# Kernel tuning notes

Measured on AMD Instinct MI355X. Metric: run time of the kernel, lower is better.

## Reference

```python
import jax, jax.numpy as jnp
import numpy as np

B, LATENT, HIDDEN, HEAD_H, OUT = 262144, 64, 512, 64, 4
EPS = 1e-5


def _layernorm(a, g, b):
    mu = jnp.mean(a, axis=-1, keepdims=True)
    var = jnp.mean(jnp.square(a - mu), axis=-1, keepdims=True)
    return (a - mu) / jnp.sqrt(var + EPS) * g + b


def _leaky(a):
    return jnp.where(a >= 0, a, 0.2 * a)


def setup_inputs() -> dict:
    key = jax.random.key(0)
    ks = jax.random.split(key, 12)
    s = lambda fan_in: 1.0 / np.sqrt(fan_in)
    return {
        "z": jax.random.normal(ks[0], (B, LATENT), dtype=jnp.float32),
        "x": jax.random.randint(ks[1], (B,), 0, 2, dtype=jnp.int32),
        "y": jax.random.randint(ks[2], (B,), 0, 2, dtype=jnp.int32),
        # encoder params (Linear stored as [in, out])
        "W1": jax.random.normal(ks[3], (LATENT, HIDDEN), dtype=jnp.float32) * s(LATENT),
        "b1": jnp.zeros((HIDDEN,), dtype=jnp.float32),
        "g1": jnp.ones((HIDDEN,), dtype=jnp.float32),
        "beta1": jnp.zeros((HIDDEN,), dtype=jnp.float32),
        "W2": jax.random.normal(ks[4], (HIDDEN, HIDDEN), dtype=jnp.float32) * s(HIDDEN),
        "b2": jnp.zeros((HIDDEN,), dtype=jnp.float32),
        "g2": jnp.ones((HIDDEN,), dtype=jnp.float32),
        "beta2": jnp.zeros((HIDDEN,), dtype=jnp.float32),
        # 4 setting-specific heads, stacked on leading axis k = 2*x + y
        "Wh1": jax.random.normal(ks[5], (4, HIDDEN, HEAD_H), dtype=jnp.float32) * s(HIDDEN),
        "bh1": jnp.zeros((4, HEAD_H), dtype=jnp.float32),
        "Wh2": jax.random.normal(ks[6], (4, HEAD_H, OUT), dtype=jnp.float32) * s(HEAD_H),
        "bh2": jnp.zeros((4, OUT), dtype=jnp.float32),
    }


def reference(z, x, y, W1, b1, g1, beta1, W2, b2, g2, beta2, Wh1, bh1, Wh2, bh2):
    # encoder: Linear -> LayerNorm -> LeakyReLU(0.2), twice
    h = _leaky(_layernorm(z @ W1 + b1, g1, beta1))          # [B, HIDDEN]
    h = _leaky(_layernorm(h @ W2 + b2, g2, beta2))          # [B, HIDDEN]
    # all 4 heads in one pass, then per-row select (equivalent to mask routing)
    t = jax.nn.relu(jnp.einsum("bh,khd->bkd", h, Wh1) + bh1)  # [B, 4, HEAD_H]
    logits_all = jnp.einsum("bkd,kdo->bko", t, Wh2) + bh2     # [B, 4, OUT]
    k = 2 * x + y                                              # head index per row
    logits = logits_all[jnp.arange(logits_all.shape[0]), k]    # [B, OUT]
    return jax.nn.softmax(logits, axis=-1)
```

## Files before the change

### kernel.cpp

```cpp
#include <hip/hip_runtime.h>

#define MT 48
#define TS 520
#define NROWS 262144
#define EPSV 1e-5f

typedef __attribute__((ext_vector_type(8))) short short8;
typedef __attribute__((ext_vector_type(4))) float floatx4;
typedef __attribute__((ext_vector_type(2))) float floatx2;
typedef __attribute__((ext_vector_type(4))) unsigned int uintx4;
typedef __attribute__((ext_vector_type(2))) unsigned int uintx2;

__device__ __forceinline__ unsigned short f2bf(float f) {
    unsigned u = __builtin_bit_cast(unsigned, f);
    u += 0x7fff + ((u >> 16) & 1);
    return (unsigned short)(u >> 16);
}
__device__ __forceinline__ float bf2f(short s) {
    unsigned u = ((unsigned)(unsigned short)s) << 16;
    return __builtin_bit_cast(float, u);
}
__device__ __forceinline__ unsigned cvtpk(float a, float b) {
    unsigned r;
    asm("v_cvt_pk_bf16_f32 %0, %1, %2" : "=v"(r) : "v"(a), "v"(b));
    return r;
}
template<int C>
__device__ __forceinline__ float dpp_add(float v) {
    int t = __builtin_amdgcn_update_dpp(0, __builtin_bit_cast(int, v), C, 0xf, 0xf, true);
    return v + __builtin_bit_cast(float, t);
}
__device__ __forceinline__ float red16(float v) {
    v = dpp_add<0x111>(v);
    v = dpp_add<0x112>(v);
    v = dpp_add<0x114>(v);
    v = dpp_add<0x118>(v);
    return v;
}

__global__ void convert_weights(const float* __restrict__ W1, const float* __restrict__ W2,
                                const float* __restrict__ Wh1, short* __restrict__ ws) {
    int idx = blockIdx.x * 256 + threadIdx.x;
    if (idx < 32768) {
        int j = idx & 7, lane = (idx >> 3) & 63, c = idx >> 9;
        int ks = c & 1, nt = (c >> 1) & 7, w = c >> 4;
        int k = ks * 32 + (lane >> 4) * 8 + j;
        int n = w * 128 + nt * 16 + (lane & 15);
        ws[idx] = (short)f2bf(W1[k * 512 + n]);
    } else if (idx < 32768 + 262144) {
        int jdx = idx - 32768;
        int j = jdx & 7, lane = (jdx >> 3) & 63, c = jdx >> 9;
        int nt = c & 7, ks = (c >> 3) & 15, w = c >> 7;
        int kp = ks * 32 + (lane >> 4) * 8 + j;
        int k  = (kp & 0x180) + ((kp & 7) << 4) + ((kp >> 3) & 15);
        int n = w * 128 + nt * 16 + (lane & 15);
        ws[idx] = (short)f2bf(W2[k * 512 + n]);
    } else if (idx < 32768 + 262144 + 131072) {
        int jdx = idx - (32768 + 262144);
        int j = jdx & 7, lane = (jdx >> 3) & 63, c = jdx >> 9;
        int nt = c & 3, ks = (c >> 2) & 15, w = c >> 6;
        int kp = ks * 32 + (lane >> 4) * 8 + j;
        int k  = (kp & 0x180) + ((kp & 7) << 4) + ((kp >> 3) & 15);
        int col = w * 64 + nt * 16 + (lane & 15);
        int kk = col >> 6, d = col & 63;
        ws[idx] = (short)f2bf(Wh1[(kk * 512 + k) * 64 + d]);
    }
}

__global__ __launch_bounds__(256, 2) void fused_kernel(
    const float* __restrict__ z, const int* __restrict__ x, const int* __restrict__ y,
    const float* __restrict__ b1, const float* __restrict__ g1, const float* __restrict__ be1,
    const float* __restrict__ b2, const float* __restrict__ g2, const float* __restrict__ be2,
    const float* __restrict__ bh1, const float* __restrict__ Wh2, const float* __restrict__ bh2,
    const short* __restrict__ ws, float* __restrict__ out)
{
    __shared__ __align__(16) short tile[MT * TS];
    __shared__ float pstats[MT][8];
    __shared__ floatx2 rstats[MT];

    int tid  = threadIdx.x;
    int wave = tid >> 6;
    int lane = tid & 63;
    int quad = lane >> 4;
    int l16  = lane & 15;
    int blk0 = blockIdx.x * MT;
    int nslab = wave * 128;

    const short* bbase1 = ws + wave * (16 * 512) + lane * 8;
    const short* bbase2 = ws + 32768 + wave * (16 * 8 * 512) + lane * 8;
    const short* bbase3 = ws + 32768 + 262144 + wave * (16 * 4 * 512) + lane * 8;

    floatx4 acc[3][8];

#pragma unroll
    for (int mt = 0; mt < 3; mt++)
#pragma unroll
        for (int nt = 0; nt < 8; nt++) acc[mt][nt] = (floatx4){0.f, 0.f, 0.f, 0.f};

    __builtin_amdgcn_s_setprio(1);
#pragma unroll
    for (int ks = 0; ks < 2; ks++) {
        short8 afr[3];
#pragma unroll
        for (int mt = 0; mt < 3; mt++) {
            int row = blk0 + mt * 16 + l16;
            row = (row < NROWS) ? row : (NROWS - 1);
            const float* zp = z + row * 64 + ks * 32 + quad * 8;
            floatx4 f0 = *(const floatx4*)zp;
            floatx4 f1 = *(const floatx4*)(zp + 4);
            uintx4 up;
            up[0] = cvtpk(f0[0], f0[1]); up[1] = cvtpk(f0[2], f0[3]);
            up[2] = cvtpk(f1[0], f1[1]); up[3] = cvtpk(f1[2], f1[3]);
            afr[mt] = __builtin_bit_cast(short8, up);
        }
#pragma unroll
        for (int nt = 0; nt < 8; nt++) {
            short8 b = *(const short8*)(bbase1 + (nt * 2 + ks) * 512);
#pragma unroll
            for (int mt = 0; mt < 3; mt++)
                acc[mt][nt] = __builtin_amdgcn_mfma_f32_16x16x32_bf16(afr[mt], b, acc[mt][nt], 0, 0, 0);
        }
    }
    __builtin_amdgcn_s_setprio(0);

    {
#pragma unroll
        for (int nt = 0; nt < 8; nt++) {
            float bv = b1[nslab + nt * 16 + l16];
#pragma unroll
            for (int mt = 0; mt < 3; mt++)
#pragma unroll
                for (int r2 = 0; r2 < 4; r2++) acc[mt][nt][r2] += bv;
        }
        float sum[3][4] = {}, sq[3][4] = {};
#pragma unroll
        for (int mt = 0; mt < 3; mt++)
#pragma unroll
            for (int nt = 0; nt < 8; nt++)
#pragma unroll
                for (int r2 = 0; r2 < 4; r2++) {
                    float v = acc[mt][nt][r2];
                    sum[mt][r2] += v; sq[mt][r2] += v * v;
                }
#pragma unroll
        for (int mt = 0; mt < 3; mt++)
#pragma unroll
            for (int r2 = 0; r2 < 4; r2++) {
                sum[mt][r2] = red16(sum[mt][r2]);
                sq[mt][r2]  = red16(sq[mt][r2]);
            }
        if (l16 == 15) {
#pragma unroll
            for (int mt = 0; mt < 3; mt++)
#pragma unroll
                for (int r2 = 0; r2 < 4; r2++) {
                    int row = mt * 16 + quad * 4 + r2;
                    *(floatx2*)&pstats[row][wave * 2] = (floatx2){sum[mt][r2], sq[mt][r2]};
                }
        }
    }
    __syncthreads();
    if (tid < MT) {
        float s = pstats[tid][0] + pstats[tid][2] + pstats[tid][4] + pstats[tid][6];
        float q = pstats[tid][1] + pstats[tid][3] + pstats[tid][5] + pstats[tid][7];
        float mean = s * (1.f / 512.f);
        float var  = q * (1.f / 512.f) - mean * mean;
        rstats[tid] = (floatx2){mean, rsqrtf(var + EPSV)};
    }
    __syncthreads();
    {
        floatx2 st[3][4];
#pragma unroll
        for (int mt = 0; mt < 3; mt++)
#pragma unroll
            for (int r2 = 0; r2 < 4; r2++) st[mt][r2] = rstats[mt * 16 + quad * 4 + r2];
        float gv[8], bev[8];
#pragma unroll
        for (int nt = 0; nt < 8; nt++) {
            int col = nslab + nt * 16 + l16;
            gv[nt] = g1[col]; bev[nt] = be1[col];
        }
#pragma unroll
        for (int mt = 0; mt < 3; mt++)
#pragma unroll
            for (int r2 = 0; r2 < 4; r2++) {
                int row = mt * 16 + quad * 4 + r2;
                float mean = st[mt][r2][0], rstd = st[mt][r2][1];
                float f[8];
#pragma unroll
                for (int nt = 0; nt < 8; nt++) {
                    float v = (acc[mt][nt][r2] - mean) * rstd * gv[nt] + bev[nt];
                    f[nt] = fmaxf(v, 0.2f * v);
                }
                uintx4 up;
                up[0] = cvtpk(f[0], f[1]); up[1] = cvtpk(f[2], f[3]);
                up[2] = cvtpk(f[4], f[5]); up[3] = cvtpk(f[6], f[7]);
                *(uintx4*)&tile[row * TS + nslab + l16 * 8] = up;
            }
    }
    __syncthreads();

#pragma unroll
    for (int mt = 0; mt < 3; mt++)
#pragma unroll
        for (int nt = 0; nt < 8; nt++) acc[mt][nt] = (floatx4){0.f, 0.f, 0.f, 0.f};

    __builtin_amdgcn_s_setprio(1);
    for (int ks = 0; ks < 16; ks++) {
        short8 afr[3];
#pragma unroll
        for (int mt = 0; mt < 3; mt++) {
            int row = mt * 16 + l16;
            afr[mt] = *(const short8*)&tile[row * TS + ks * 32 + quad * 8];
        }
#pragma unroll
        for (int nt = 0; nt < 8; nt++) {
            short8 b = *(const short8*)(bbase2 + (ks * 8 + nt) * 512);
#pragma unroll
            for (int mt = 0; mt < 3; mt++)
                acc[mt][nt] = __builtin_amdgcn_mfma_f32_16x16x32_bf16(afr[mt], b, acc[mt][nt], 0, 0, 0);
        }
    }
    __builtin_amdgcn_s_setprio(0);
    {
#pragma unroll
        for (int nt = 0; nt < 8; nt++) {
            float bv = b2[nslab + nt * 16 + l16];
#pragma unroll
            for (int mt = 0; mt < 3; mt++)
#pragma unroll
                for (int r2 = 0; r2 < 4; r2++) acc[mt][nt][r2] += bv;
        }
        float sum[3][4] = {}, sq[3][4] = {};
#pragma unroll
        for (int mt = 0; mt < 3; mt++)
#pragma unroll
            for (int nt = 0; nt < 8; nt++)
#pragma unroll
                for (int r2 = 0; r2 < 4; r2++) {
                    float v = acc[mt][nt][r2];
                    sum[mt][r2] += v; sq[mt][r2] += v * v;
                }
#pragma unroll
        for (int mt = 0; mt < 3; mt++)
#pragma unroll
            for (int r2 = 0; r2 < 4; r2++) {
                sum[mt][r2] = red16(sum[mt][r2]);
                sq[mt][r2]  = red16(sq[mt][r2]);
            }
        if (l16 == 15) {
#pragma unroll
            for (int mt = 0; mt < 3; mt++)
#pragma unroll
                for (int r2 = 0; r2 < 4; r2++) {
                    int row = mt * 16 + quad * 4 + r2;
                    *(floatx2*)&pstats[row][wave * 2] = (floatx2){sum[mt][r2], sq[mt][r2]};
                }
        }
    }
    __syncthreads();
    if (tid < MT) {
        float s = pstats[tid][0] + pstats[tid][2] + pstats[tid][4] + pstats[tid][6];
        float q = pstats[tid][1] + pstats[tid][3] + pstats[tid][5] + pstats[tid][7];
        float mean = s * (1.f / 512.f);
        float var  = q * (1.f / 512.f) - mean * mean;
        rstats[tid] = (floatx2){mean, rsqrtf(var + EPSV)};
    }
    __syncthreads();
    {
        floatx2 st[3][4];
#pragma unroll
        for (int mt = 0; mt < 3; mt++)
#pragma unroll
            for (int r2 = 0; r2 < 4; r2++) st[mt][r2] = rstats[mt * 16 + quad * 4 + r2];
        float gv[8], bev[8];
#pragma unroll
        for (int nt = 0; nt < 8; nt++) {
            int col = nslab + nt * 16 + l16;
            gv[nt] = g2[col]; bev[nt] = be2[col];
        }
#pragma unroll
        for (int mt = 0; mt < 3; mt++)
#pragma unroll
            for (int r2 = 0; r2 < 4; r2++) {
                int row = mt * 16 + quad * 4 + r2;
                float mean = st[mt][r2][0], rstd = st[mt][r2][1];
                float f[8];
#pragma unroll
                for (int nt = 0; nt < 8; nt++) {
                    float v = (acc[mt][nt][r2] - mean) * rstd * gv[nt] + bev[nt];
                    f[nt] = fmaxf(v, 0.2f * v);
                }
                uintx4 up;
                up[0] = cvtpk(f[0], f[1]); up[1] = cvtpk(f[2], f[3]);
                up[2] = cvtpk(f[4], f[5]); up[3] = cvtpk(f[6], f[7]);
                *(uintx4*)&tile[row * TS + nslab + l16 * 8] = up;
            }
    }
    __syncthreads();

#pragma unroll
    for (int mt = 0; mt < 3; mt++)
#pragma unroll
        for (int nt = 0; nt < 4; nt++) acc[mt][nt] = (floatx4){0.f, 0.f, 0.f, 0.f};

    __builtin_amdgcn_s_setprio(1);
    for (int ks = 0; ks < 16; ks++) {
        short8 afr[3];
#pragma unroll
        for (int mt = 0; mt < 3; mt++) {
            int row = mt * 16 + l16;
            afr[mt] = *(const short8*)&tile[row * TS + ks * 32 + quad * 8];
        }
#pragma unroll
        for (int nt = 0; nt < 4; nt++) {
            short8 b = *(const short8*)(bbase3 + (ks * 4 + nt) * 512);
#pragma unroll
            for (int mt = 0; mt < 3; mt++)
                acc[mt][nt] = __builtin_amdgcn_mfma_f32_16x16x32_bf16(afr[mt], b, acc[mt][nt], 0, 0, 0);
        }
    }
    __builtin_amdgcn_s_setprio(0);
    __syncthreads();
    {
        float bh1v[4];
#pragma unroll
        for (int nt = 0; nt < 4; nt++) bh1v[nt] = bh1[wave * 64 + nt * 16 + l16];
#pragma unroll
        for (int mt = 0; mt < 3; mt++)
#pragma unroll
            for (int r2 = 0; r2 < 4; r2++) {
                int row = mt * 16 + quad * 4 + r2;
                float f[4];
#pragma unroll
                for (int nt = 0; nt < 4; nt++) {
                    float v = acc[mt][nt][r2] + bh1v[nt];
                    f[nt] = (v > 0.f) ? v : 0.f;
                }
                uintx2 up = {cvtpk(f[0], f[1]), cvtpk(f[2], f[3])};
                *(uintx2*)&tile[row * TS + wave * 64 + l16 * 4] = up;
            }
    }
    __syncthreads();

    {
        int r = tid >> 2, is = tid & 3;
        if (r < MT) {
            int grow = blk0 + r;
            int gsafe = (grow < NROWS) ? grow : (NROWS - 1);
            int kk = 2 * x[gsafe] + y[gsafe];
            const short* tp = &tile[r * TS + kk * 64 + is * 16];
            short8 ta = *(const short8*)tp;
            short8 tb = *(const short8*)(tp + 8);
            const float* wp = Wh2 + kk * 256;
            float lg0 = 0.f, lg1 = 0.f, lg2 = 0.f, lg3 = 0.f;
#pragma unroll
            for (int e = 0; e < 8; e++) {
                int d0 = (e & 3) * 16 + 4 * is + (e >> 2);
                float t0 = bf2f(ta[e]);
                floatx4 w0 = *(const floatx4*)(wp + d0 * 4);
                float t1 = bf2f(tb[e]);
                floatx4 w1 = *(const floatx4*)(wp + (d0 + 2) * 4);
                lg0 += t0 * w0[0] + t1 * w1[0];
                lg1 += t0 * w0[1] + t1 * w1[1];
                lg2 += t0 * w0[2] + t1 * w1[2];
                lg3 += t0 * w0[3] + t1 * w1[3];
            }
#pragma unroll
            for (int off = 1; off < 4; off <<= 1) {
                lg0 += __shfl_xor(lg0, off, 64);
                lg1 += __shfl_xor(lg1, off, 64);
                lg2 += __shfl_xor(lg2, off, 64);
                lg3 += __shfl_xor(lg3, off, 64);
            }
            if (is == 0 && grow < NROWS) {
                lg0 += bh2[kk * 4 + 0]; lg1 += bh2[kk * 4 + 1];
                lg2 += bh2[kk * 4 + 2]; lg3 += bh2[kk * 4 + 3];
                float m = fmaxf(fmaxf(lg0, lg1), fmaxf(lg2, lg3));
                float e0 = __expf(lg0 - m), e1 = __expf(lg1 - m);
                float e2 = __expf(lg2 - m), e3 = __expf(lg3 - m);
                float inv = 1.f / (e0 + e1 + e2 + e3);
                floatx4 o = {e0 * inv, e1 * inv, e2 * inv, e3 * inv};
                *(floatx4*)(out + grow * 4) = o;
            }
        }
    }
}

extern "C" void kernel_launch(void* const* d_in, const int* in_sizes, int n_in,
                              void* d_out, int out_size, void* d_ws, size_t ws_size,
                              hipStream_t stream) {
    const float* z   = (const float*)d_in[0];
    const int*   x   = (const int*)d_in[1];
    const int*   y   = (const int*)d_in[2];
    const float* W1  = (const float*)d_in[3];
    const float* b1  = (const float*)d_in[4];
    const float* g1  = (const float*)d_in[5];
    const float* be1 = (const float*)d_in[6];
    const float* W2  = (const float*)d_in[7];
    const float* b2  = (const float*)d_in[8];
    const float* g2  = (const float*)d_in[9];
    const float* be2 = (const float*)d_in[10];
    const float* Wh1 = (const float*)d_in[11];
    const float* bh1 = (const float*)d_in[12];
    const float* Wh2 = (const float*)d_in[13];
    const float* bh2 = (const float*)d_in[14];
    short* ws = (short*)d_ws;
    float* out = (float*)d_out;

    hipLaunchKernelGGL(convert_weights, dim3(1664), dim3(256), 0, stream, W1, W2, Wh1, ws);
    hipLaunchKernelGGL(fused_kernel, dim3((NROWS + MT - 1) / MT), dim3(256), 0, stream,
                       z, x, y, b1, g1, be1, b2, g2, be2, bh1, Wh2, bh2,
                       (const short*)ws, out);
}
```

Baseline: 401.0 us.

## Restructure fused MLP so each wave owns full rows with LDS-staged shared weights

The kernel is reorganised so each of 8 waves owns 16 rows across all 512 columns, with 128 rows per 512-thread block. Weights are streamed through a double-buffered LDS buffer using global_load_lds, and that buffer is shared by all waves. LayerNorm statistics are now reduced within a wave, which removes the cross-wave pstats/rstats synchronisation, and epilogue math uses packed f32 instructions with an XOR-swizzled per-wave scratch layout. This cuts the global weight traffic per row and the block-level barriers for stats. In exchange it adds a __syncthreads per weight chunk, needs 128 accumulator VGPRs per thread, and drops the bounds guards because it assumes NROWS is divisible by 128.

```diff
diff --git a/kernel.cpp b/kernel.cpp
--- a/kernel.cpp
+++ b/kernel.cpp
@@ -1,15 +1,15 @@
 #include <hip/hip_runtime.h>
 
-#define MT 48
-#define TS 520
 #define NROWS 262144
+#define MT 128
+#define NBLK (NROWS / MT)
 #define EPSV 1e-5f
 
 typedef __attribute__((ext_vector_type(8))) short short8;
+typedef __attribute__((ext_vector_type(4))) short shortx4;
 typedef __attribute__((ext_vector_type(4))) float floatx4;
 typedef __attribute__((ext_vector_type(2))) float floatx2;
 typedef __attribute__((ext_vector_type(4))) unsigned int uintx4;
-typedef __attribute__((ext_vector_type(2))) unsigned int uintx2;
 
 __device__ __forceinline__ unsigned short f2bf(float f) {
     unsigned u = __builtin_bit_cast(unsigned, f);
@@ -24,6 +24,15 @@
     unsigned r;
     asm("v_cvt_pk_bf16_f32 %0, %1, %2" : "=v"(r) : "v"(a), "v"(b));
     return r;
+}
+__device__ __forceinline__ floatx2 pk_add(floatx2 a, floatx2 b) {
+    floatx2 d; asm("v_pk_add_f32 %0, %1, %2" : "=v"(d) : "v"(a), "v"(b)); return d;
+}
+__device__ __forceinline__ floatx2 pk_mul(floatx2 a, floatx2 b) {
+    floatx2 d; asm("v_pk_mul_f32 %0, %1, %2" : "=v"(d) : "v"(a), "v"(b)); return d;
+}
+__device__ __forceinline__ floatx2 pk_fma(floatx2 a, floatx2 b, floatx2 c) {
+    floatx2 d; asm("v_pk_fma_f32 %0, %1, %2, %3" : "=v"(d) : "v"(a), "v"(b), "v"(c)); return d;
 }
 template<int C>
 __device__ __forceinline__ float dpp_add(float v) {
@@ -37,352 +46,314 @@
     v = dpp_add<0x118>(v);
     return v;
 }
+__device__ __forceinline__ float bcast15(float v) {
+    return __builtin_bit_cast(float,
+        __builtin_amdgcn_ds_swizzle(__builtin_bit_cast(int, v), 0x01F0));
+}
+__device__ __forceinline__ void gload16(const short* g, short* l) {
+    __builtin_amdgcn_global_load_lds(
+        (const __attribute__((address_space(1))) unsigned int*)g,
+        (__attribute__((address_space(3))) unsigned int*)l, 16, 0, 0);
+}
 
 __global__ void convert_weights(const float* __restrict__ W1, const float* __restrict__ W2,
                                 const float* __restrict__ Wh1, short* __restrict__ ws) {
     int idx = blockIdx.x * 256 + threadIdx.x;
     if (idx < 32768) {
         int j = idx & 7, lane = (idx >> 3) & 63, c = idx >> 9;
-        int ks = c & 1, nt = (c >> 1) & 7, w = c >> 4;
-        int k = ks * 32 + (lane >> 4) * 8 + j;
-        int n = w * 128 + nt * 16 + (lane & 15);
+        int ntl = c & 7, ks = (c >> 3) & 1, ncg = c >> 4;
+        int q = lane >> 4, l16 = lane & 15;
+        int k = ks * 32 + q * 8 + j;
+        int n = ncg * 128 + ntl * 16 + l16;
         ws[idx] = (short)f2bf(W1[k * 512 + n]);
     } else if (idx < 32768 + 262144) {
         int jdx = idx - 32768;
         int j = jdx & 7, lane = (jdx >> 3) & 63, c = jdx >> 9;
-        int nt = c & 7, ks = (c >> 3) & 15, w = c >> 7;
-        int kp = ks * 32 + (lane >> 4) * 8 + j;
-        int k  = (kp & 0x180) + ((kp & 7) << 4) + ((kp >> 3) & 15);
-        int n = w * 128 + nt * 16 + (lane & 15);
+        int ntl = c & 7, ks = (c >> 3) & 15, ncg = c >> 7;
+        int q = lane >> 4, l16 = lane & 15;
+        int k = (q * 8 + j) * 16 + ks;
+        int n = ncg * 128 + ntl * 16 + l16;
         ws[idx] = (short)f2bf(W2[k * 512 + n]);
     } else if (idx < 32768 + 262144 + 131072) {
         int jdx = idx - (32768 + 262144);
         int j = jdx & 7, lane = (jdx >> 3) & 63, c = jdx >> 9;
-        int nt = c & 3, ks = (c >> 2) & 15, w = c >> 6;
-        int kp = ks * 32 + (lane >> 4) * 8 + j;
-        int k  = (kp & 0x180) + ((kp & 7) << 4) + ((kp >> 3) & 15);
-        int col = w * 64 + nt * 16 + (lane & 15);
-        int kk = col >> 6, d = col & 63;
-        ws[idx] = (short)f2bf(Wh1[(kk * 512 + k) * 64 + d]);
-    }
-}
-
-__global__ __launch_bounds__(256, 2) void fused_kernel(
+        int ntl = c & 7, ks = (c >> 3) & 15, ncg = c >> 7;
+        int q = lane >> 4, l16 = lane & 15;
+        int k = (q * 8 + j) * 16 + ks;
+        int d = ncg * 128 + ntl * 16 + l16;
+        int kk = d >> 6, dd = d & 63;
+        ws[idx] = (short)f2bf(Wh1[(kk * 512 + k) * 64 + dd]);
+    }
+}
+
+__global__ __launch_bounds__(512, 2) void fused_kernel(
     const float* __restrict__ z, const int* __restrict__ x, const int* __restrict__ y,
     const float* __restrict__ b1, const float* __restrict__ g1, const float* __restrict__ be1,
     const float* __restrict__ b2, const float* __restrict__ g2, const float* __restrict__ be2,
     const float* __restrict__ bh1, const float* __restrict__ Wh2, const float* __restrict__ bh2,
     const short* __restrict__ ws, float* __restrict__ out)
 {
-    __shared__ __align__(16) short tile[MT * TS];
-    __shared__ float pstats[MT][8];
-    __shared__ floatx2 rstats[MT];
+    __shared__ __align__(16) short scr[8 * 16 * 512];
+    __shared__ __align__(16) short bbuf[2][8 * 512];
 
     int tid  = threadIdx.x;
     int wave = tid >> 6;
     int lane = tid & 63;
     int quad = lane >> 4;
     int l16  = lane & 15;
-    int blk0 = blockIdx.x * MT;
-    int nslab = wave * 128;
-
-    const short* bbase1 = ws + wave * (16 * 512) + lane * 8;
-    const short* bbase2 = ws + 32768 + wave * (16 * 8 * 512) + lane * 8;
-    const short* bbase3 = ws + 32768 + 262144 + wave * (16 * 4 * 512) + lane * 8;
-
-    floatx4 acc[3][8];
-
-#pragma unroll
-    for (int mt = 0; mt < 3; mt++)
-#pragma unroll
-        for (int nt = 0; nt < 8; nt++) acc[mt][nt] = (floatx4){0.f, 0.f, 0.f, 0.f};
-
-    __builtin_amdgcn_s_setprio(1);
+    int row0 = blockIdx.x * MT + wave * 16;
+
+    short* myscr = scr + wave * (16 * 512);
+
+    floatx4 acc[32];
+
+    short8 azfr[2];
 #pragma unroll
     for (int ks = 0; ks < 2; ks++) {
-        short8 afr[3];
-#pragma unroll
-        for (int mt = 0; mt < 3; mt++) {
-            int row = blk0 + mt * 16 + l16;
-            row = (row < NROWS) ? row : (NROWS - 1);
-            const float* zp = z + row * 64 + ks * 32 + quad * 8;
-            floatx4 f0 = *(const floatx4*)zp;
-            floatx4 f1 = *(const floatx4*)(zp + 4);
-            uintx4 up;
-            up[0] = cvtpk(f0[0], f0[1]); up[1] = cvtpk(f0[2], f0[3]);
-            up[2] = cvtpk(f1[0], f1[1]); up[3] = cvtpk(f1[2], f1[3]);
-            afr[mt] = __builtin_bit_cast(short8, up);
-        }
-#pragma unroll
-        for (int nt = 0; nt < 8; nt++) {
-            short8 b = *(const short8*)(bbase1 + (nt * 2 + ks) * 512);
-#pragma unroll
-            for (int mt = 0; mt < 3; mt++)
-                acc[mt][nt] = __builtin_amdgcn_mfma_f32_16x16x32_bf16(afr[mt], b, acc[mt][nt], 0, 0, 0);
-        }
-    }
-    __builtin_amdgcn_s_setprio(0);
+        const float* zp = z + (row0 + l16) * 64 + ks * 32 + quad * 8;
+        floatx4 f0 = *(const floatx4*)zp;
+        floatx4 f1 = *(const floatx4*)(zp + 4);
+        uintx4 up;
+        up[0] = cvtpk(f0[0], f0[1]); up[1] = cvtpk(f0[2], f0[3]);
+        up[2] = cvtpk(f1[0], f1[1]); up[3] = cvtpk(f1[2], f1[3]);
+        azfr[ks] = __builtin_bit_cast(short8, up);
+    }
+
+    gload16(ws + tid * 8, &bbuf[0][tid * 8]);
+    __syncthreads();
+    const short* wsp = ws + 4096;
+    int cur = 0;
+
+#pragma unroll
+    for (int nt = 0; nt < 32; nt++) acc[nt] = (floatx4){0.f, 0.f, 0.f, 0.f};
+#pragma unroll
+    for (int c = 0; c < 8; c++) {
+        int ncg = c >> 1, ks = c & 1;
+        gload16(wsp + tid * 8, &bbuf[cur ^ 1][tid * 8]);
+        wsp += 4096;
+#pragma unroll
+        for (int ntl = 0; ntl < 8; ntl++) {
+            short8 b = *(const short8*)&bbuf[cur][ntl * 512 + lane * 8];
+            acc[ncg * 8 + ntl] =
+                __builtin_amdgcn_mfma_f32_16x16x32_bf16(azfr[ks], b, acc[ncg * 8 + ntl], 0, 0, 0);
+        }
+        __syncthreads();
+        cur ^= 1;
+    }
 
     {
-#pragma unroll
-        for (int nt = 0; nt < 8; nt++) {
-            float bv = b1[nslab + nt * 16 + l16];
-#pragma unroll
-            for (int mt = 0; mt < 3; mt++)
-#pragma unroll
-                for (int r2 = 0; r2 < 4; r2++) acc[mt][nt][r2] += bv;
-        }
-        float sum[3][4] = {}, sq[3][4] = {};
-#pragma unroll
-        for (int mt = 0; mt < 3; mt++)
-#pragma unroll
-            for (int nt = 0; nt < 8; nt++)
+        floatx2 s2[2] = {}, q2[2] = {};
+#pragma unroll
+        for (int nt = 0; nt < 32; nt++) {
+            float bv = b1[nt * 16 + l16];
+            floatx2 bb = {bv, bv};
+            floatx2 v01 = {acc[nt][0], acc[nt][1]};
+            floatx2 v23 = {acc[nt][2], acc[nt][3]};
+            v01 = pk_add(v01, bb); v23 = pk_add(v23, bb);
+            acc[nt][0] = v01[0]; acc[nt][1] = v01[1];
+            acc[nt][2] = v23[0]; acc[nt][3] = v23[1];
+            s2[0] = pk_add(s2[0], v01); q2[0] = pk_fma(v01, v01, q2[0]);
+            s2[1] = pk_add(s2[1], v23); q2[1] = pk_fma(v23, v23, q2[1]);
+        }
+#pragma unroll
+        for (int pr = 0; pr < 2; pr++) {
+            s2[pr][0] = red16(s2[pr][0]); s2[pr][1] = red16(s2[pr][1]);
+            q2[pr][0] = red16(q2[pr][0]); q2[pr][1] = red16(q2[pr][1]);
+        }
+        float nm[4], rs[4];
+#pragma unroll
+        for (int r2 = 0; r2 < 4; r2++) {
+            float s = bcast15(s2[r2 >> 1][r2 & 1]);
+            float q = bcast15(q2[r2 >> 1][r2 & 1]);
+            float mean = s * (1.f / 512.f);
+            float var  = q * (1.f / 512.f) - mean * mean;
+            nm[r2] = -mean; rs[r2] = rsqrtf(var + EPSV);
+        }
+#pragma unroll
+        for (int seg = 0; seg < 4; seg++) {
+            uintx4 upv[4];
+#pragma unroll
+            for (int sl = 0; sl < 4; sl++) {
+                int nt = seg * 8 + sl * 2;
+                floatx2 gg = {g1[nt * 16 + l16],  g1[nt * 16 + 16 + l16]};
+                floatx2 bb = {be1[nt * 16 + l16], be1[nt * 16 + 16 + l16]};
 #pragma unroll
                 for (int r2 = 0; r2 < 4; r2++) {
-                    float v = acc[mt][nt][r2];
-                    sum[mt][r2] += v; sq[mt][r2] += v * v;
+                    floatx2 v = {acc[nt][r2], acc[nt + 1][r2]};
+                    floatx2 t = pk_mul(pk_add(v, (floatx2){nm[r2], nm[r2]}),
+                                       (floatx2){rs[r2], rs[r2]});
+                    floatx2 f = pk_fma(t, gg, bb);
+                    upv[r2][sl] = cvtpk(fmaxf(f[0], 0.2f * f[0]), fmaxf(f[1], 0.2f * f[1]));
                 }
-#pragma unroll
-        for (int mt = 0; mt < 3; mt++)
+            }
 #pragma unroll
             for (int r2 = 0; r2 < 4; r2++) {
-                sum[mt][r2] = red16(sum[mt][r2]);
-                sq[mt][r2]  = red16(sq[mt][r2]);
-            }
-        if (l16 == 15) {
-#pragma unroll
-            for (int mt = 0; mt < 3; mt++)
+                int row = quad * 4 + r2;
+                int cb = l16 * 4 + seg;
+                *(uintx4*)&myscr[row * 512 + ((cb ^ (row & 7)) << 3)] = upv[r2];
+            }
+        }
+    }
+
+#pragma unroll
+    for (int nt = 0; nt < 32; nt++) acc[nt] = (floatx4){0.f, 0.f, 0.f, 0.f};
+#pragma unroll
+    for (int ncg = 0; ncg < 4; ncg++) {
+        for (int ks = 0; ks < 16; ks++) {
+            gload16(wsp + tid * 8, &bbuf[cur ^ 1][tid * 8]);
+            wsp += 4096;
+            short8 afr = *(const short8*)&myscr[l16 * 512 + (((ks * 4 + quad) ^ (l16 & 7)) << 3)];
+#pragma unroll
+            for (int ntl = 0; ntl < 8; ntl++) {
+                short8 b = *(const short8*)&bbuf[cur][ntl * 512 + lane * 8];
+                acc[ncg * 8 + ntl] =
+                    __builtin_amdgcn_mfma_f32_16x16x32_bf16(afr, b, acc[ncg * 8 + ntl], 0, 0, 0);
+            }
+            __syncthreads();
+            cur ^= 1;
+        }
+    }
+
+    {
+        floatx2 s2[2] = {}, q2[2] = {};
+#pragma unroll
+        for (int nt = 0; nt < 32; nt++) {
+            float bv = b2[nt * 16 + l16];
+            floatx2 bb = {bv, bv};
+            floatx2 v01 = {acc[nt][0], acc[nt][1]};
+            floatx2 v23 = {acc[nt][2], acc[nt][3]};
+            v01 = pk_add(v01, bb); v23 = pk_add(v23, bb);
+            acc[nt][0] = v01[0]; acc[nt][1] = v01[1];
+            acc[nt][2] = v23[0]; acc[nt][3] = v23[1];
+            s2[0] = pk_add(s2[0], v01); q2[0] = pk_fma(v01, v01, q2[0]);
+            s2[1] = pk_add(s2[1], v23); q2[1] = pk_fma(v23, v23, q2[1]);
+        }
+#pragma unroll
+        for (int pr = 0; pr < 2; pr++) {
+            s2[pr][0] = red16(s2[pr][0]); s2[pr][1] = red16(s2[pr][1]);
+            q2[pr][0] = red16(q2[pr][0]); q2[pr][1] = red16(q2[pr][1]);
+        }
+        float nm[4], rs[4];
+#pragma unroll
+        for (int r2 = 0; r2 < 4; r2++) {
+            float s = bcast15(s2[r2 >> 1][r2 & 1]);
+            float q = bcast15(q2[r2 >> 1][r2 & 1]);
+            float mean = s * (1.f / 512.f);
+            float var  = q * (1.f / 512.f) - mean * mean;
+            nm[r2] = -mean; rs[r2] = rsqrtf(var + EPSV);
+        }
+#pragma unroll
+        for (int seg = 0; seg < 4; seg++) {
+            uintx4 upv[4];
+#pragma unroll
+            for (int sl = 0; sl < 4; sl++) {
+                int nt = seg * 8 + sl * 2;
+                floatx2 gg = {g2[nt * 16 + l16],  g2[nt * 16 + 16 + l16]};
+                floatx2 bb = {be2[nt * 16 + l16], be2[nt * 16 + 16 + l16]};
 #pragma unroll
                 for (int r2 = 0; r2 < 4; r2++) {
-                    int row = mt * 16 + quad * 4 + r2;
-                    *(floatx2*)&pstats[row][wave * 2] = (floatx2){sum[mt][r2], sq[mt][r2]};
+                    floatx2 v = {acc[nt][r2], acc[nt + 1][r2]};
+                    floatx2 t = pk_mul(pk_add(v, (floatx2){nm[r2], nm[r2]}),
+                                       (floatx2){rs[r2], rs[r2]});
+                    floatx2 f = pk_fma(t, gg, bb);
+                    upv[r2][sl] = cvtpk(fmaxf(f[0], 0.2f * f[0]), fmaxf(f[1], 0.2f * f[1]));
                 }
-        }
-    }
-    __syncthreads();
-    if (tid < MT) {
-        float s = pstats[tid][0] + pstats[tid][2] + pstats[tid][4] + pstats[tid][6];
-        float q = pstats[tid][1] + pstats[tid][3] + pstats[tid][5] + pstats[tid][7];
-        float mean = s * (1.f / 512.f);
-        float var  = q * (1.f / 512.f) - mean * mean;
-        rstats[tid] = (floatx2){mean, rsqrtf(var + EPSV)};
-    }
-    __syncthreads();
+            }
+#pragma unroll
+            for (int r2 = 0; r2 < 4; r2++) {
+                int row = quad * 4 + r2;
+                int cb = l16 * 4 + seg;
+                *(uintx4*)&myscr[row * 512 + ((cb ^ (row & 7)) << 3)] = upv[r2];
+            }
+        }
+    }
+
+#pragma unroll
+    for (int nt = 0; nt < 16; nt++) acc[nt] = (floatx4){0.f, 0.f, 0.f, 0.f};
+#pragma unroll
+    for (int ncg = 0; ncg < 2; ncg++) {
+        for (int ks = 0; ks < 16; ks++) {
+            if (!(ncg == 1 && ks == 15)) {
+                gload16(wsp + tid * 8, &bbuf[cur ^ 1][tid * 8]);
+                wsp += 4096;
+            }
+            short8 afr = *(const short8*)&myscr[l16 * 512 + (((ks * 4 + quad) ^ (l16 & 7)) << 3)];
+#pragma unroll
+            for (int ntl = 0; ntl < 8; ntl++) {
+                short8 b = *(const short8*)&bbuf[cur][ntl * 512 + lane * 8];
+                acc[ncg * 8 + ntl] =
+                    __builtin_amdgcn_mfma_f32_16x16x32_bf16(afr, b, acc[ncg * 8 + ntl], 0, 0, 0);
+            }
+            __syncthreads();
+            cur ^= 1;
+        }
+    }
+
     {
-        floatx2 st[3][4];
-#pragma unroll
-        for (int mt = 0; mt < 3; mt++)
-#pragma unroll
-            for (int r2 = 0; r2 < 4; r2++) st[mt][r2] = rstats[mt * 16 + quad * 4 + r2];
-        float gv[8], bev[8];
-#pragma unroll
-        for (int nt = 0; nt < 8; nt++) {
-            int col = nslab + nt * 16 + l16;
-            gv[nt] = g1[col]; bev[nt] = be1[col];
-        }
-#pragma unroll
-        for (int mt = 0; mt < 3; mt++)
+#pragma unroll
+        for (int seg = 0; seg < 2; seg++) {
+            uintx4 upv[4];
+#pragma unroll
+            for (int sl = 0; sl < 4; sl++) {
+                int nt = seg * 8 + sl * 2;
+                floatx2 bb = {bh1[nt * 16 + l16], bh1[nt * 16 + 16 + l16]};
+#pragma unroll
+                for (int r2 = 0; r2 < 4; r2++) {
+                    floatx2 v = pk_add((floatx2){acc[nt][r2], acc[nt + 1][r2]}, bb);
+                    upv[r2][sl] = cvtpk(fmaxf(v[0], 0.f), fmaxf(v[1], 0.f));
+                }
+            }
 #pragma unroll
             for (int r2 = 0; r2 < 4; r2++) {
-                int row = mt * 16 + quad * 4 + r2;
-                float mean = st[mt][r2][0], rstd = st[mt][r2][1];
-                float f[8];
-#pragma unroll
-                for (int nt = 0; nt < 8; nt++) {
-                    float v = (acc[mt][nt][r2] - mean) * rstd * gv[nt] + bev[nt];
-                    f[nt] = fmaxf(v, 0.2f * v);
-                }
-                uintx4 up;
-                up[0] = cvtpk(f[0], f[1]); up[1] = cvtpk(f[2], f[3]);
-                up[2] = cvtpk(f[4], f[5]); up[3] = cvtpk(f[6], f[7]);
-                *(uintx4*)&tile[row * TS + nslab + l16 * 8] = up;
-            }
-    }
-    __syncthreads();
-
-#pragma unroll
-    for (int mt = 0; mt < 3; mt++)
-#pragma unroll
-        for (int nt = 0; nt < 8; nt++) acc[mt][nt] = (floatx4){0.f, 0.f, 0.f, 0.f};
-
-    __builtin_amdgcn_s_setprio(1);
-    for (int ks = 0; ks < 16; ks++) {
-        short8 afr[3];
-#pragma unroll
-        for (int mt = 0; mt < 3; mt++) {
-            int row = mt * 16 + l16;
-            afr[mt] = *(const short8*)&tile[row * TS + ks * 32 + quad * 8];
-        }
-#pragma unroll
-        for (int nt = 0; nt < 8; nt++) {
-            short8 b = *(const short8*)(bbase2 + (ks * 8 + nt) * 512);
-#pragma unroll
-            for (int mt = 0; mt < 3; mt++)
-                acc[mt][nt] = __builtin_amdgcn_mfma_f32_16x16x32_bf16(afr[mt], b, acc[mt][nt], 0, 0, 0);
-        }
-    }
-    __builtin_amdgcn_s_setprio(0);
+                int row = quad * 4 + r2;
+                int cb = l16 * 2 + seg;
+                *(uintx4*)&myscr[row * 512 + ((cb ^ (row & 7)) << 3)] = upv[r2];
+            }
+        }
+    }
+
     {
-#pragma unroll
-        for (int nt = 0; nt < 8; nt++) {
-            float bv = b2[nslab + nt * 16 + l16];
-#pragma unroll
-            for (int mt = 0; mt < 3; mt++)
-#pragma unroll
-                for (int r2 = 0; r2 < 4; r2++) acc[mt][nt][r2] += bv;
-        }
-        float sum[3][4] = {}, sq[3][4] = {};
-#pragma unroll
-        for (int mt = 0; mt < 3; mt++)
-#pragma unroll
-            for (int nt = 0; nt < 8; nt++)
-#pragma unroll
-                for (int r2 = 0; r2 < 4; r2++) {
-                    float v = acc[mt][nt][r2];
-                    sum[mt][r2] += v; sq[mt][r2] += v * v;
-                }
-#pragma unroll
-        for (int mt = 0; mt < 3; mt++)
-#pragma unroll
-            for (int r2 = 0; r2 < 4; r2++) {
-                sum[mt][r2] = red16(sum[mt][r2]);
-                sq[mt][r2]  = red16(sq[mt][r2]);
-            }
-        if (l16 == 15) {
-#pragma unroll
-            for (int mt = 0; mt < 3; mt++)
-#pragma unroll
-                for (int r2 = 0; r2 < 4; r2++) {
-                    int row = mt * 16 + quad * 4 + r2;
-                    *(floatx2*)&pstats[row][wave * 2] = (floatx2){sum[mt][r2], sq[mt][r2]};
-                }
-        }
-    }
-    __syncthreads();
-    if (tid < MT) {
-        float s = pstats[tid][0] + pstats[tid][2] + pstats[tid][4] + pstats[tid][6];
-        float q = pstats[tid][1] + pstats[tid][3] + pstats[tid][5] + pstats[tid][7];
-        float mean = s * (1.f / 512.f);
-        float var  = q * (1.f / 512.f) - mean * mean;
-        rstats[tid] = (floatx2){mean, rsqrtf(var + EPSV)};
-    }
-    __syncthreads();
-    {
-        floatx2 st[3][4];
-#pragma unroll
-        for (int mt = 0; mt < 3; mt++)
-#pragma unroll
-            for (int r2 = 0; r2 < 4; r2++) st[mt][r2] = rstats[mt * 16 + quad * 4 + r2];
-        float gv[8], bev[8];
-#pragma unroll
-        for (int nt = 0; nt < 8; nt++) {
-            int col = nslab + nt * 16 + l16;
-            gv[nt] = g2[col]; bev[nt] = be2[col];
-        }
-#pragma unroll
-        for (int mt = 0; mt < 3; mt++)
-#pragma unroll
-            for (int r2 = 0; r2 < 4; r2++) {
-                int row = mt * 16 + quad * 4 + r2;
-                float mean = st[mt][r2][0], rstd = st[mt][r2][1];
-                float f[8];
-#pragma unroll
-                for (int nt = 0; nt < 8; nt++) {
-                    float v = (acc[mt][nt][r2] - mean) * rstd * gv[nt] + bev[nt];
-                    f[nt] = fmaxf(v, 0.2f * v);
-                }
-                uintx4 up;
-                up[0] = cvtpk(f[0], f[1]); up[1] = cvtpk(f[2], f[3]);
-                up[2] = cvtpk(f[4], f[5]); up[3] = cvtpk(f[6], f[7]);
-                *(uintx4*)&tile[row * TS + nslab + l16 * 8] = up;
-            }
-    }
-    __syncthreads();
-
-#pragma unroll
-    for (int mt = 0; mt < 3; mt++)
-#pragma unroll
-        for (int nt = 0; nt < 4; nt++) acc[mt][nt] = (floatx4){0.f, 0.f, 0.f, 0.f};
-
-    __builtin_amdgcn_s_setprio(1);
-    for (int ks = 0; ks < 16; ks++) {
-        short8 afr[3];
-#pragma unroll
-        for (int mt = 0; mt < 3; mt++) {
-            int row = mt * 16 + l16;
-            afr[mt] = *(const short8*)&tile[row * TS + ks * 32 + quad * 8];
-        }
-#pragma unroll
-        for (int nt = 0; nt < 4; nt++) {
-            short8 b = *(const short8*)(bbase3 + (ks * 4 + nt) * 512);
-#pragma unroll
-            for (int mt = 0; mt < 3; mt++)
-                acc[mt][nt] = __builtin_amdgcn_mfma_f32_16x16x32_bf16(afr[mt], b, acc[mt][nt], 0, 0, 0);
-        }
-    }
-    __builtin_amdgcn_s_setprio(0);
-    __syncthreads();
-    {
-        float bh1v[4];
-#pragma unroll
-        for (int nt = 0; nt < 4; nt++) bh1v[nt] = bh1[wave * 64 + nt * 16 + l16];
-#pragma unroll
-        for (int mt = 0; mt < 3; mt++)
-#pragma unroll
-            for (int r2 = 0; r2 < 4; r2++) {
-                int row = mt * 16 + quad * 4 + r2;
-                float f[4];
-#pragma unroll
-                for (int nt = 0; nt < 4; nt++) {
-                    float v = acc[mt][nt][r2] + bh1v[nt];
-                    f[nt] = (v > 0.f) ? v : 0.f;
-                }
-                uintx2 up = {cvtpk(f[0], f[1]), cvtpk(f[2], f[3])};
-                *(uintx2*)&tile[row * TS + wave * 64 + l16 * 4] = up;
-            }
-    }
-    __syncthreads();
-
-    {
-        int r = tid >> 2, is = tid & 3;
-        if (r < MT) {
-            int grow = blk0 + r;
-            int gsafe = (grow < NROWS) ? grow : (NROWS - 1);
-            int kk = 2 * x[gsafe] + y[gsafe];
-            const short* tp = &tile[r * TS + kk * 64 + is * 16];
-            short8 ta = *(const short8*)tp;
-            short8 tb = *(const short8*)(tp + 8);
-            const float* wp = Wh2 + kk * 256;
-            float lg0 = 0.f, lg1 = 0.f, lg2 = 0.f, lg3 = 0.f;
-#pragma unroll
-            for (int e = 0; e < 8; e++) {
-                int d0 = (e & 3) * 16 + 4 * is + (e >> 2);
-                float t0 = bf2f(ta[e]);
-                floatx4 w0 = *(const floatx4*)(wp + d0 * 4);
-                float t1 = bf2f(tb[e]);
-                floatx4 w1 = *(const floatx4*)(wp + (d0 + 2) * 4);
-                lg0 += t0 * w0[0] + t1 * w1[0];
-                lg1 += t0 * w0[1] + t1 * w1[1];
-                lg2 += t0 * w0[2] + t1 * w1[2];
-                lg3 += t0 * w0[3] + t1 * w1[3];
-            }
-#pragma unroll
-            for (int off = 1; off < 4; off <<= 1) {
-                lg0 += __shfl_xor(lg0, off, 64);
-                lg1 += __shfl_xor(lg1, off, 64);
-                lg2 += __shfl_xor(lg2, off, 64);
-                lg3 += __shfl_xor(lg3, off, 64);
-            }
-            if (is == 0 && grow < NROWS) {
-                lg0 += bh2[kk * 4 + 0]; lg1 += bh2[kk * 4 + 1];
-                lg2 += bh2[kk * 4 + 2]; lg3 += bh2[kk * 4 + 3];
-                float m = fmaxf(fmaxf(lg0, lg1), fmaxf(lg2, lg3));
-                float e0 = __expf(lg0 - m), e1 = __expf(lg1 - m);
-                float e2 = __expf(lg2 - m), e3 = __expf(lg3 - m);
-                float inv = 1.f / (e0 + e1 + e2 + e3);
-                floatx4 o = {e0 * inv, e1 * inv, e2 * inv, e3 * inv};
-                *(floatx4*)(out + grow * 4) = o;
-            }
+        int rl = lane >> 2, is = lane & 3;
+        int grow = row0 + rl;
+        int kk = 2 * x[grow] + y[grow];
+        float tv[16];
+#pragma unroll
+        for (int m = 0; m < 4; m++) {
+            int k3 = (4 * is + m) * 16 + kk * 4;
+            int cb = k3 >> 3;
+            int off = k3 & 7;
+            shortx4 t4 = *(const shortx4*)&myscr[rl * 512 + ((cb ^ (rl & 7)) << 3) + off];
+            tv[m * 4 + 0] = bf2f(t4[0]); tv[m * 4 + 1] = bf2f(t4[1]);
+            tv[m * 4 + 2] = bf2f(t4[2]); tv[m * 4 + 3] = bf2f(t4[3]);
+        }
+        const float* wp = Wh2 + kk * 256;
+        float lg0 = 0.f, lg1 = 0.f, lg2 = 0.f, lg3 = 0.f;
+#pragma unroll
+        for (int m = 0; m < 4; m++)
+#pragma unroll
+            for (int ntl = 0; ntl < 4; ntl++) {
+                int dd = ntl * 16 + 4 * is + m;
+                floatx4 w = *(const floatx4*)(wp + dd * 4);
+                float t = tv[m * 4 + ntl];
+                lg0 += t * w[0]; lg1 += t * w[1];
+                lg2 += t * w[2]; lg3 += t * w[3];
+            }
+#pragma unroll
+        for (int off = 1; off < 4; off <<= 1) {
+            lg0 += __shfl_xor(lg0, off, 64);
+            lg1 += __shfl_xor(lg1, off, 64);
+            lg2 += __shfl_xor(lg2, off, 64);
+            lg3 += __shfl_xor(lg3, off, 64);
+        }
+        if (is == 0) {
+            lg0 += bh2[kk * 4 + 0]; lg1 += bh2[kk * 4 + 1];
+            lg2 += bh2[kk * 4 + 2]; lg3 += bh2[kk * 4 + 3];
+            float mmax = fmaxf(fmaxf(lg0, lg1), fmaxf(lg2, lg3));
+            float e0 = __expf(lg0 - mmax), e1 = __expf(lg1 - mmax);
+            float e2 = __expf(lg2 - mmax), e3 = __expf(lg3 - mmax);
+            float inv = 1.f / (e0 + e1 + e2 + e3);
+            floatx4 o = {e0 * inv, e1 * inv, e2 * inv, e3 * inv};
+            *(floatx4*)(out + grow * 4) = o;
         }
     }
 }
@@ -409,7 +380,7 @@
     float* out = (float*)d_out;
 
     hipLaunchKernelGGL(convert_weights, dim3(1664), dim3(256), 0, stream, W1, W2, Wh1, ws);
-    hipLaunchKernelGGL(fused_kernel, dim3((NROWS + MT - 1) / MT), dim3(256), 0, stream,
+    hipLaunchKernelGGL(fused_kernel, dim3(NBLK), dim3(512), 0, stream,
                        z, x, y, b1, g1, be1, b2, g2, be2, bh1, Wh2, bh2,
                        (const short*)ws, out);
 }
```

Result: slower. 486.9 us (+21.4%).
